# Performance work log

Measured on AMD Instinct MI355X. Metric: run time of the kernel, lower is better.

The kernel has to match this reference:

```python
import jax, jax.numpy as jnp
import numpy as np

K = 64  # hardcoded in MAN.__init__
D_DRUG = 128
D_PROT = 128


def setup_inputs() -> dict:
    key = jax.random.key(0)
    ks = jax.random.split(key, 7)
    B, Ld, Lp = 64, 512, 1024

    def xavier(k, shape):
        fan_in, fan_out = shape[-1], shape[-2]
        std = (2.0 / (fan_in + fan_out)) ** 0.5
        return jax.random.normal(k, shape, dtype=jnp.float32) * std

    return {
        "drug": jax.random.normal(ks[0], (B, Ld, D_DRUG), dtype=jnp.float32),
        "target": jax.random.normal(ks[1], (B, Lp, D_PROT), dtype=jnp.float32),
        "W_b": xavier(ks[2], (D_PROT, D_DRUG)),
        "W_x": xavier(ks[3], (K, D_DRUG)),
        "W_p": xavier(ks[4], (K, D_PROT)),
        "w_hx": xavier(ks[5], (K, 1)),
        "w_hp": xavier(ks[6], (K, 1)),
    }


def reference(drug, target, W_b, W_x, W_p, w_hx, w_hp):
    # drug:   [B, Ld, Dd] ; target: [B, Lp, Dp]
    d = jnp.swapaxes(drug, 1, 2)            # [B, Dd, Ld]  (drug.permute(0,2,1))
    tT = jnp.swapaxes(target, 1, 2)         # [B, Dp, Lp]

    # C = tanh(target @ (W_b @ d))  -> [B, Lp, Ld]
    C = jnp.tanh(jnp.einsum('bpe,ed,bdl->bpl', target, W_b, d))

    Wx_d = jnp.einsum('kd,bdl->bkl', W_x, d)     # [B, k, Ld]
    Wp_t = jnp.einsum('ke,bep->bkp', W_p, tT)    # [B, k, Lp]

    H_c = jnp.tanh(Wx_d + jnp.einsum('bkp,bpl->bkl', Wp_t, C))   # [B, k, Ld]
    H_p = jnp.tanh(Wp_t + jnp.einsum('bkl,bpl->bkp', Wx_d, C))   # [B, k, Lp]

    a_c = jax.nn.softmax(jnp.einsum('k,bkl->bl', w_hx[:, 0], H_c), axis=-1)  # [B, Ld]
    a_p = jax.nn.softmax(jnp.einsum('k,bkp->bp', w_hp[:, 0], H_p), axis=-1)  # [B, Lp]

    c = jnp.einsum('bl,bld->bd', a_c, drug)      # [B, Dd]
    p = jnp.einsum('bp,bpe->be', a_p, target)    # [B, Dp]
    return (c, p)
```

## Files before the change

kernel.cpp:

```cpp
#include <hip/hip_runtime.h>
#include <hip/hip_bf16.h>
#include <math.h>

#define NB 64
#define LD 512
#define LP 1024
#define DD 128
#define KK 64

using half8 = __attribute__((ext_vector_type(8))) _Float16;
using half4 = __attribute__((ext_vector_type(4))) _Float16;
using f32x4 = __attribute__((ext_vector_type(4))) float;

__device__ __forceinline__ float ftanh(float x) {
    float e = __expf(2.0f * x);
    return 1.0f - 2.0f * __builtin_amdgcn_rcpf(e + 1.0f);
}

__global__ void k_conv(const float* __restrict__ in, _Float16* __restrict__ out, int n) {
    int i = (blockIdx.x * blockDim.x + threadIdx.x) * 4;
    int stride = gridDim.x * blockDim.x * 4;
    for (; i < n; i += stride) {
        float4 v = *reinterpret_cast<const float4*>(in + i);
        half4 h;
        h.x = (_Float16)v.x; h.y = (_Float16)v.y; h.z = (_Float16)v.z; h.w = (_Float16)v.w;
        *reinterpret_cast<half4*>(out + i) = h;
    }
}

__global__ void k_prep(const float* __restrict__ Wb, _Float16* __restrict__ WbT,
                       const float* __restrict__ Wx, _Float16* __restrict__ Wx_h,
                       const float* __restrict__ Wp, _Float16* __restrict__ Wp_h)
{
    int bid = blockIdx.x, tid = threadIdx.x;
    if (bid < 64) {
        int t = bid * 256 + tid;
        int d = t >> 7, e = t & 127;
        WbT[t] = (_Float16)Wb[e * 128 + d];
    } else {
        const float* src = (bid < 72) ? Wx : Wp;
        _Float16* dst = (bid < 72) ? Wx_h : Wp_h;
        int i = ((bid & 7) * 256 + tid) * 4;
        float4 v = *reinterpret_cast<const float4*>(src + i);
        half4 h;
        h.x = (_Float16)v.x; h.y = (_Float16)v.y; h.z = (_Float16)v.z; h.w = (_Float16)v.w;
        *reinterpret_cast<half4*>(dst + i) = h;
    }
}

__global__ void k_sentinel(float* out) {
    if (threadIdx.x == 0 && blockIdx.x == 0) out[0] = 1000.0f;
}

__global__ __launch_bounds__(256)
void k_gemm3(const _Float16* __restrict__ drug_h, const _Float16* __restrict__ targ_h,
             const _Float16* __restrict__ WbT_h, const _Float16* __restrict__ Wx_h,
             const _Float16* __restrict__ Wp_h,
             _Float16* __restrict__ tb_h, _Float16* __restrict__ Wxd_h,
             _Float16* __restrict__ Wpt_h)
{
    __shared__ alignas(16) _Float16 smem[64 * 72 + 128 * 72];
    _Float16* As = smem;
    _Float16* Bs = smem + 64 * 72;

    int bid = blockIdx.x;
    const _Float16 *A, *Bm;
    _Float16* Out;
    long sA, sB, sOut;
    int N, tilesN, t;
    const int Kd = 128;
    if (bid < 256)      { A = Wx_h;  sA = 0;            Bm = drug_h; sB = (long)LD * DD; Out = Wxd_h; sOut = (long)KK * LD; N = LD;  tilesN = 4; t = bid; }
    else if (bid < 768) { A = Wp_h;  sA = 0;            Bm = targ_h; sB = (long)LP * DD; Out = Wpt_h; sOut = (long)KK * LP; N = LP;  tilesN = 8; t = bid - 256; }
    else                { A = targ_h; sA = (long)LP * DD; Bm = WbT_h; sB = 0;            Out = tb_h;  sOut = (long)LP * DD; N = 128; tilesN = 1; t = bid - 768; }

    int tpb = (tilesN == 1) ? 16 : tilesN;
    int b = t / tpb;
    int q = t % tpb;
    int m0 = (tilesN == 1) ? q * 64 : 0;
    int n0 = (tilesN == 1) ? 0 : q * 128;

    const _Float16* Ab = A + (long)b * sA;
    const _Float16* Bb = Bm + (long)b * sB;

    int tid = threadIdx.x;
    int lane = tid & 63;
    int wid = tid >> 6;
    int wm = wid & 1, wn = wid >> 1;

    f32x4 acc[2][4];
#pragma unroll
    for (int i = 0; i < 2; i++)
#pragma unroll
        for (int j = 0; j < 4; j++) acc[i][j] = (f32x4)(0.0f);

    for (int k0 = 0; k0 < Kd; k0 += 64) {
#pragma unroll
        for (int i = 0; i < 2; i++) {
            int c = tid + i * 256;
            int row = c >> 3, col = c & 7;
            int4 v = *reinterpret_cast<const int4*>(Ab + (long)(m0 + row) * Kd + k0 + col * 8);
            *reinterpret_cast<int4*>(&As[row * 72 + col * 8]) = v;
        }
#pragma unroll
        for (int i = 0; i < 4; i++) {
            int c = tid + i * 256;
            int row = c >> 3, col = c & 7;
            int4 v = *reinterpret_cast<const int4*>(Bb + (long)(n0 + row) * Kd + k0 + col * 8);
            *reinterpret_cast<int4*>(&Bs[row * 72 + col * 8]) = v;
        }
        __syncthreads();
#pragma unroll
        for (int kk = 0; kk < 64; kk += 32) {
            int klane = kk + 8 * (lane >> 4);
            half8 af[2], bfr[4];
#pragma unroll
            for (int fm = 0; fm < 2; fm++)
                af[fm] = *reinterpret_cast<const half8*>(&As[(wm * 32 + fm * 16 + (lane & 15)) * 72 + klane]);
#pragma unroll
            for (int fn = 0; fn < 4; fn++)
                bfr[fn] = *reinterpret_cast<const half8*>(&Bs[(wn * 64 + fn * 16 + (lane & 15)) * 72 + klane]);
#pragma unroll
            for (int fm = 0; fm < 2; fm++)
#pragma unroll
                for (int fn = 0; fn < 4; fn++)
                    acc[fm][fn] = __builtin_amdgcn_mfma_f32_16x16x32_f16(af[fm], bfr[fn], acc[fm][fn], 0, 0, 0);
        }
        __syncthreads();
    }

    long ob = (long)b * sOut;
#pragma unroll
    for (int fm = 0; fm < 2; fm++)
#pragma unroll
        for (int fn = 0; fn < 4; fn++)
#pragma unroll
            for (int r = 0; r < 4; r++) {
                int row = m0 + wm * 32 + fm * 16 + (lane >> 4) * 4 + r;
                int col = n0 + wn * 64 + fn * 16 + (lane & 15);
                Out[ob + (long)row * N + col] = (_Float16)acc[fm][fn][r];
            }
}

__global__ __launch_bounds__(256)
void k_score_fused(const _Float16* __restrict__ drug_h, const _Float16* __restrict__ tb_h,
                   const _Float16* __restrict__ Wxd_h, const _Float16* __restrict__ Wpt_h,
                   const float* __restrict__ whx, const float* __restrict__ whp,
                   float* __restrict__ sc_c, float* __restrict__ sc_p)
{
    __shared__ alignas(16) _Float16 Ss[64 * 136];
    __shared__ alignas(16) _Float16 Ws[64 * 72];
    __shared__ alignas(16) _Float16 Cts[64 * 72];
    __shared__ float sred[8 * 64];
    __shared__ float wsh[64];

    int P = blockIdx.x;
    int tid = threadIdx.x;
    int lane = tid & 63;
    int wid = tid >> 6;
    int wm = wid & 1, wn = wid >> 1;

    int b, n0, nsteps, Ntot, sW;
    const _Float16 *R, *S, *W, *Add;
    const float* wv;
    float* out;
    if (P < 512) {
        int x = P & 7, j = P >> 3;
        b = x * 8 + (j >> 3);
        n0 = (j & 7) * 64;
        R = drug_h + (long)b * (LD * DD);
        S = tb_h   + (long)b * (LP * DD);
        W = Wpt_h  + (long)b * (KK * LP);  sW = LP;
        Add = Wxd_h + (long)b * (KK * LD); Ntot = LD;
        nsteps = LP / 64; wv = whx; out = sc_c + (long)b * LD;
    } else {
        int Q = P - 512;
        int x = Q & 7, j = Q >> 3;
        b = x * 8 + (j >> 4);
        n0 = (j & 15) * 64;
        R = tb_h   + (long)b * (LP * DD);
        S = drug_h + (long)b * (LD * DD);
        W = Wxd_h  + (long)b * (KK * LD);  sW = LD;
        Add = Wpt_h + (long)b * (KK * LP); Ntot = LP;
        nsteps = LD / 64; wv = whp; out = sc_p + (long)b * LP;
    }

    half8 af[2][4];
#pragma unroll
    for (int fm = 0; fm < 2; fm++)
#pragma unroll
        for (int kk = 0; kk < 4; kk++) {
            int row = n0 + wm * 32 + fm * 16 + (lane & 15);
            int col = kk * 32 + 8 * (lane >> 4);
            af[fm][kk] = *reinterpret_cast<const half8*>(R + (long)row * DD + col);
        }
    if (tid < 64) wsh[tid] = wv[tid];

    f32x4 acc2[2][2];
#pragma unroll
    for (int i = 0; i < 2; i++)
#pragma unroll
        for (int j = 0; j < 2; j++) acc2[i][j] = (f32x4)(0.0f);

    for (int s = 0; s < nsteps; s++) {
        __syncthreads();
#pragma unroll
        for (int i = 0; i < 4; i++) {
            int c = tid + i * 256;
            int row = c >> 4, col8 = (c & 15) * 8;
            int4 v = *reinterpret_cast<const int4*>(S + (long)(s * 64 + row) * DD + col8);
            *reinterpret_cast<int4*>(&Ss[row * 136 + col8]) = v;
        }
#pragma unroll
        for (int i = 0; i < 2; i++) {
            int c = tid + i * 256;
            int row = c >> 3, col8 = (c & 7) * 8;
            int4 v = *reinterpret_cast<const int4*>(W + (long)row * sW + s * 64 + col8);
            *reinterpret_cast<int4*>(&Ws[row * 72 + col8]) = v;
        }
        __syncthreads();

        f32x4 a1[2][2];
#pragma unroll
        for (int i = 0; i < 2; i++)
#pragma unroll
            for (int j = 0; j < 2; j++) a1[i][j] = (f32x4)(0.0f);
#pragma unroll
        for (int kk = 0; kk < 4; kk++) {
            int klane = kk * 32 + 8 * (lane >> 4);
            half8 bf[2];
#pragma unroll
            for (int fn = 0; fn < 2; fn++)
                bf[fn] = *reinterpret_cast<const half8*>(&Ss[(wn * 32 + fn * 16 + (lane & 15)) * 136 + klane]);
#pragma unroll
            for (int fn = 0; fn < 2; fn++)
#pragma unroll
                for (int fm = 0; fm < 2; fm++)
                    a1[fn][fm] = __builtin_amdgcn_mfma_f32_16x16x32_f16(bf[fn], af[fm][kk], a1[fn][fm], 0, 0, 0);
        }
#pragma unroll
        for (int fn = 0; fn < 2; fn++)
#pragma unroll
            for (int fm = 0; fm < 2; fm++) {
                int res   = wm * 32 + fm * 16 + (lane & 15);
                int strm0 = wn * 32 + fn * 16 + 4 * (lane >> 4);
                half4 hv;
                hv.x = (_Float16)ftanh(a1[fn][fm][0]);
                hv.y = (_Float16)ftanh(a1[fn][fm][1]);
                hv.z = (_Float16)ftanh(a1[fn][fm][2]);
                hv.w = (_Float16)ftanh(a1[fn][fm][3]);
                *reinterpret_cast<half4*>(&Cts[res * 72 + strm0]) = hv;
            }
        __syncthreads();

#pragma unroll
        for (int kk = 0; kk < 2; kk++) {
            int klane = kk * 32 + 8 * (lane >> 4);
            half8 aw[2], bf2[2];
#pragma unroll
            for (int fm = 0; fm < 2; fm++)
                aw[fm] = *reinterpret_cast<const half8*>(&Ws[(wm * 32 + fm * 16 + (lane & 15)) * 72 + klane]);
#pragma unroll
            for (int fn = 0; fn < 2; fn++)
                bf2[fn] = *reinterpret_cast<const half8*>(&Cts[(wn * 32 + fn * 16 + (lane & 15)) * 72 + klane]);
#pragma unroll
            for (int fm = 0; fm < 2; fm++)
#pragma unroll
                for (int fn = 0; fn < 2; fn++)
                    acc2[fm][fn] = __builtin_amdgcn_mfma_f32_16x16x32_f16(aw[fm], bf2[fn], acc2[fm][fn], 0, 0, 0);
        }
    }

    float ps[2] = {0.f, 0.f};
#pragma unroll
    for (int fm = 0; fm < 2; fm++)
#pragma unroll
        for (int fn = 0; fn < 2; fn++)
#pragma unroll
            for (int r = 0; r < 4; r++) {
                int k   = wm * 32 + fm * 16 + (lane >> 4) * 4 + r;
                int col = wn * 32 + fn * 16 + (lane & 15);
                float v = ftanh(acc2[fm][fn][r] + (float)Add[(long)k * Ntot + n0 + col]);
                ps[fn] += wsh[k] * v;
            }
#pragma unroll
    for (int fn = 0; fn < 2; fn++)
        sred[(wm * 4 + (lane >> 4)) * 64 + wn * 32 + fn * 16 + (lane & 15)] = ps[fn];
    __syncthreads();
    if (tid < 64) {
        float sacc = 0.f;
#pragma unroll
        for (int j = 0; j < 8; j++) sacc += sred[j * 64 + tid];
        out[n0 + tid] = sacc;
    }
}

__device__ __forceinline__ float wred_max(float v) {
#pragma unroll
    for (int off = 32; off > 0; off >>= 1) v = fmaxf(v, __shfl_xor(v, off, 64));
    return v;
}
__device__ __forceinline__ float wred_sum(float v) {
#pragma unroll
    for (int off = 32; off > 0; off >>= 1) v += __shfl_xor(v, off, 64);
    return v;
}

__global__ __launch_bounds__(1024)
void k_soft(const float* __restrict__ scc, const float* __restrict__ scp,
            float* __restrict__ ac, float* __restrict__ ap)
{
    __shared__ float r16[16];
    int b = blockIdx.x, tid = threadIdx.x;
    int lane = tid & 63, wid = tid >> 6;

    float s = (tid < 512) ? scc[b * 512 + tid] : -3.4e38f;
    float m = wred_max(s);
    if (lane == 0) r16[wid] = m;
    __syncthreads();
    m = r16[0];
#pragma unroll
    for (int i = 1; i < 16; i++) m = fmaxf(m, r16[i]);
    float e = (tid < 512) ? __expf(s - m) : 0.f;
    __syncthreads();
    float t = wred_sum(e);
    if (lane == 0) r16[wid] = t;
    __syncthreads();
    float sum = 0.f;
#pragma unroll
    for (int i = 0; i < 16; i++) sum += r16[i];
    if (tid < 512) ac[b * 512 + tid] = e * __builtin_amdgcn_rcpf(sum);
    __syncthreads();

    float s2 = scp[b * 1024 + tid];
    float m2 = wred_max(s2);
    if (lane == 0) r16[wid] = m2;
    __syncthreads();
    m2 = r16[0];
#pragma unroll
    for (int i = 1; i < 16; i++) m2 = fmaxf(m2, r16[i]);
    float e2 = __expf(s2 - m2);
    __syncthreads();
    float t2 = wred_sum(e2);
    if (lane == 0) r16[wid] = t2;
    __syncthreads();
    float sum2 = 0.f;
#pragma unroll
    for (int i = 0; i < 16; i++) sum2 += r16[i];
    ap[b * 1024 + tid] = e2 * __builtin_amdgcn_rcpf(sum2);
}

__global__ __launch_bounds__(512)
void k_wsum(const _Float16* __restrict__ drug_h, const _Float16* __restrict__ targ_h,
            const float* __restrict__ ac, const float* __restrict__ ap,
            float* __restrict__ out)
{
    __shared__ float ash[1024];
    __shared__ float red[32 * 128];
    int b = blockIdx.x, side = blockIdx.y;
    int L = side ? LP : LD;
    const _Float16* X = side ? targ_h : drug_h;
    const float* a = side ? ap : ac;
    float* ob = out + side * 8192 + b * 128;
    int tid = threadIdx.x;

    for (int i = tid; i < L; i += 512) ash[i] = a[(long)b * L + i];
    __syncthreads();

    int col8 = tid & 15, rg = tid >> 4;
    float accv[8];
#pragma unroll
    for (int j = 0; j < 8; j++) accv[j] = 0.f;
    const _Float16* Xb = X + (long)b * L * 128;
    for (int l = rg; l < L; l += 32) {
        half8 v = *reinterpret_cast<const half8*>(&Xb[l * 128 + col8 * 8]);
        float av = ash[l];
#pragma unroll
        for (int j = 0; j < 8; j++) accv[j] += av * (float)v[j];
    }
#pragma unroll
    for (int j = 0; j < 8; j++) red[rg * 128 + col8 * 8 + j] = accv[j];
    __syncthreads();
    if (tid < 128) {
        float s = 0.f;
#pragma unroll
        for (int g = 0; g < 32; g++) s += red[g * 128 + tid];
        ob[tid] = s;
    }
}

extern "C" void kernel_launch(void* const* d_in, const int* in_sizes, int n_in,
                              void* d_out, int out_size, void* d_ws, size_t ws_size,
                              hipStream_t stream) {
    (void)in_sizes; (void)n_in; (void)out_size;
    const float* drug   = (const float*)d_in[0];
    const float* target = (const float*)d_in[1];
    const float* Wb     = (const float*)d_in[2];
    const float* Wx     = (const float*)d_in[3];
    const float* Wp     = (const float*)d_in[4];
    const float* whx    = (const float*)d_in[5];
    const float* whp    = (const float*)d_in[6];

    char* w = (char*)d_ws;
    size_t off = 0;
    auto takeb = [&](size_t bytes) {
        void* p = (void*)(w + off);
        off += (bytes + 255) & ~(size_t)255;
        return p;
    };
    _Float16* drug_h = (_Float16*)takeb((size_t)NB * LD * DD * 2);
    _Float16* targ_h = (_Float16*)takeb((size_t)NB * LP * DD * 2);
    _Float16* WbT_h  = (_Float16*)takeb(128 * 128 * 2);
    _Float16* Wx_h   = (_Float16*)takeb(64 * 128 * 2);
    _Float16* Wp_h   = (_Float16*)takeb(64 * 128 * 2);
    _Float16* tb_h   = (_Float16*)takeb((size_t)NB * LP * DD * 2);
    _Float16* Wxd_h  = (_Float16*)takeb((size_t)NB * KK * LD * 2);
    _Float16* Wpt_h  = (_Float16*)takeb((size_t)NB * KK * LP * 2);
    float*    sc_c   = (float*)takeb((size_t)NB * LD * 4);
    float*    sc_p   = (float*)takeb((size_t)NB * LP * 4);
    float*    a_c    = (float*)takeb((size_t)NB * LD * 4);
    float*    a_p    = (float*)takeb((size_t)NB * LP * 4);

    if (off > ws_size) {
        k_sentinel<<<1, 64, 0, stream>>>((float*)d_out);
        return;
    }

    k_conv<<<1024, 256, 0, stream>>>(drug,   drug_h, NB * LD * DD);
    k_conv<<<1024, 256, 0, stream>>>(target, targ_h, NB * LP * DD);
    k_prep<<<80, 256, 0, stream>>>(Wb, WbT_h, Wx, Wx_h, Wp, Wp_h);

    k_gemm3<<<dim3(1792), 256, 0, stream>>>(
        drug_h, targ_h, WbT_h, Wx_h, Wp_h, tb_h, Wxd_h, Wpt_h);

    k_score_fused<<<dim3(512 + 1024), 256, 0, stream>>>(
        drug_h, tb_h, Wxd_h, Wpt_h, whx, whp, sc_c, sc_p);

    k_soft<<<NB, 1024, 0, stream>>>(sc_c, sc_p, a_c, a_p);
    k_wsum<<<dim3(NB, 2), 512, 0, stream>>>(drug_h, targ_h, a_c, a_p, (float*)d_out);
}
```

Baseline: 102.5 us.

## Double per-block output tile in fused score kernel to reuse streamed tiles

New measurement: 87.84 us. 1.17x faster.

```diff
diff --git a/kernel.cpp b/kernel.cpp
--- a/kernel.cpp
+++ b/kernel.cpp
@@ -141,7 +141,7 @@
             }
 }
 
-__global__ __launch_bounds__(256)
+__global__ __launch_bounds__(256, 3)
 void k_score_fused(const _Float16* __restrict__ drug_h, const _Float16* __restrict__ tb_h,
                    const _Float16* __restrict__ Wxd_h, const _Float16* __restrict__ Wpt_h,
                    const float* __restrict__ whx, const float* __restrict__ whp,
@@ -149,8 +149,8 @@
 {
     __shared__ alignas(16) _Float16 Ss[64 * 136];
     __shared__ alignas(16) _Float16 Ws[64 * 72];
-    __shared__ alignas(16) _Float16 Cts[64 * 72];
-    __shared__ float sred[8 * 64];
+    __shared__ alignas(16) _Float16 Cts[128 * 72];
+    __shared__ float sred[8 * 128];
     __shared__ float wsh[64];
 
     int P = blockIdx.x;
@@ -163,20 +163,20 @@
     const _Float16 *R, *S, *W, *Add;
     const float* wv;
     float* out;
-    if (P < 512) {
+    if (P < 256) {
         int x = P & 7, j = P >> 3;
-        b = x * 8 + (j >> 3);
-        n0 = (j & 7) * 64;
+        b = x * 8 + (j >> 2);
+        n0 = (j & 3) * 128;
         R = drug_h + (long)b * (LD * DD);
         S = tb_h   + (long)b * (LP * DD);
         W = Wpt_h  + (long)b * (KK * LP);  sW = LP;
         Add = Wxd_h + (long)b * (KK * LD); Ntot = LD;
         nsteps = LP / 64; wv = whx; out = sc_c + (long)b * LD;
     } else {
-        int Q = P - 512;
+        int Q = P - 256;
         int x = Q & 7, j = Q >> 3;
-        b = x * 8 + (j >> 4);
-        n0 = (j & 15) * 64;
+        b = x * 8 + (j >> 3);
+        n0 = (j & 7) * 128;
         R = tb_h   + (long)b * (LP * DD);
         S = drug_h + (long)b * (LD * DD);
         W = Wxd_h  + (long)b * (KK * LD);  sW = LD;
@@ -184,22 +184,22 @@
         nsteps = LD / 64; wv = whp; out = sc_p + (long)b * LP;
     }
 
-    half8 af[2][4];
-#pragma unroll
-    for (int fm = 0; fm < 2; fm++)
+    half8 af[4][4];
+#pragma unroll
+    for (int fm = 0; fm < 4; fm++)
 #pragma unroll
         for (int kk = 0; kk < 4; kk++) {
-            int row = n0 + wm * 32 + fm * 16 + (lane & 15);
+            int row = n0 + wm * 64 + fm * 16 + (lane & 15);
             int col = kk * 32 + 8 * (lane >> 4);
             af[fm][kk] = *reinterpret_cast<const half8*>(R + (long)row * DD + col);
         }
     if (tid < 64) wsh[tid] = wv[tid];
 
-    f32x4 acc2[2][2];
+    f32x4 acc2[2][4];
 #pragma unroll
     for (int i = 0; i < 2; i++)
 #pragma unroll
-        for (int j = 0; j < 2; j++) acc2[i][j] = (f32x4)(0.0f);
+        for (int j = 0; j < 4; j++) acc2[i][j] = (f32x4)(0.0f);
 
     for (int s = 0; s < nsteps; s++) {
         __syncthreads();
@@ -219,11 +219,11 @@
         }
         __syncthreads();
 
-        f32x4 a1[2][2];
+        f32x4 a1[2][4];
 #pragma unroll
         for (int i = 0; i < 2; i++)
 #pragma unroll
-            for (int j = 0; j < 2; j++) a1[i][j] = (f32x4)(0.0f);
+            for (int j = 0; j < 4; j++) a1[i][j] = (f32x4)(0.0f);
 #pragma unroll
         for (int kk = 0; kk < 4; kk++) {
             int klane = kk * 32 + 8 * (lane >> 4);
@@ -234,14 +234,14 @@
 #pragma unroll
             for (int fn = 0; fn < 2; fn++)
 #pragma unroll
-                for (int fm = 0; fm < 2; fm++)
+                for (int fm = 0; fm < 4; fm++)
                     a1[fn][fm] = __builtin_amdgcn_mfma_f32_16x16x32_f16(bf[fn], af[fm][kk], a1[fn][fm], 0, 0, 0);
         }
 #pragma unroll
         for (int fn = 0; fn < 2; fn++)
 #pragma unroll
-            for (int fm = 0; fm < 2; fm++) {
-                int res   = wm * 32 + fm * 16 + (lane & 15);
+            for (int fm = 0; fm < 4; fm++) {
+                int res   = wm * 64 + fm * 16 + (lane & 15);
                 int strm0 = wn * 32 + fn * 16 + 4 * (lane >> 4);
                 half4 hv;
                 hv.x = (_Float16)ftanh(a1[fn][fm][0]);
@@ -255,41 +255,41 @@
 #pragma unroll
         for (int kk = 0; kk < 2; kk++) {
             int klane = kk * 32 + 8 * (lane >> 4);
-            half8 aw[2], bf2[2];
-#pragma unroll
-            for (int fm = 0; fm < 2; fm++)
-                aw[fm] = *reinterpret_cast<const half8*>(&Ws[(wm * 32 + fm * 16 + (lane & 15)) * 72 + klane]);
-#pragma unroll
-            for (int fn = 0; fn < 2; fn++)
-                bf2[fn] = *reinterpret_cast<const half8*>(&Cts[(wn * 32 + fn * 16 + (lane & 15)) * 72 + klane]);
-#pragma unroll
-            for (int fm = 0; fm < 2; fm++)
-#pragma unroll
-                for (int fn = 0; fn < 2; fn++)
-                    acc2[fm][fn] = __builtin_amdgcn_mfma_f32_16x16x32_f16(aw[fm], bf2[fn], acc2[fm][fn], 0, 0, 0);
-        }
-    }
-
-    float ps[2] = {0.f, 0.f};
-#pragma unroll
-    for (int fm = 0; fm < 2; fm++)
-#pragma unroll
-        for (int fn = 0; fn < 2; fn++)
+            half8 aw[2], bf2[4];
+#pragma unroll
+            for (int fm2 = 0; fm2 < 2; fm2++)
+                aw[fm2] = *reinterpret_cast<const half8*>(&Ws[(wm * 32 + fm2 * 16 + (lane & 15)) * 72 + klane]);
+#pragma unroll
+            for (int fn2 = 0; fn2 < 4; fn2++)
+                bf2[fn2] = *reinterpret_cast<const half8*>(&Cts[(wn * 64 + fn2 * 16 + (lane & 15)) * 72 + klane]);
+#pragma unroll
+            for (int fm2 = 0; fm2 < 2; fm2++)
+#pragma unroll
+                for (int fn2 = 0; fn2 < 4; fn2++)
+                    acc2[fm2][fn2] = __builtin_amdgcn_mfma_f32_16x16x32_f16(aw[fm2], bf2[fn2], acc2[fm2][fn2], 0, 0, 0);
+        }
+    }
+
+    float ps[4] = {0.f, 0.f, 0.f, 0.f};
+#pragma unroll
+    for (int fm2 = 0; fm2 < 2; fm2++)
+#pragma unroll
+        for (int fn2 = 0; fn2 < 4; fn2++)
 #pragma unroll
             for (int r = 0; r < 4; r++) {
-                int k   = wm * 32 + fm * 16 + (lane >> 4) * 4 + r;
-                int col = wn * 32 + fn * 16 + (lane & 15);
-                float v = ftanh(acc2[fm][fn][r] + (float)Add[(long)k * Ntot + n0 + col]);
-                ps[fn] += wsh[k] * v;
+                int k   = wm * 32 + fm2 * 16 + (lane >> 4) * 4 + r;
+                int col = wn * 64 + fn2 * 16 + (lane & 15);
+                float v = ftanh(acc2[fm2][fn2][r] + (float)Add[(long)k * Ntot + n0 + col]);
+                ps[fn2] += wsh[k] * v;
             }
 #pragma unroll
-    for (int fn = 0; fn < 2; fn++)
-        sred[(wm * 4 + (lane >> 4)) * 64 + wn * 32 + fn * 16 + (lane & 15)] = ps[fn];
-    __syncthreads();
-    if (tid < 64) {
+    for (int fn2 = 0; fn2 < 4; fn2++)
+        sred[(wm * 4 + (lane >> 4)) * 128 + wn * 64 + fn2 * 16 + (lane & 15)] = ps[fn2];
+    __syncthreads();
+    if (tid < 128) {
         float sacc = 0.f;
 #pragma unroll
-        for (int j = 0; j < 8; j++) sacc += sred[j * 64 + tid];
+        for (int j = 0; j < 8; j++) sacc += sred[j * 128 + tid];
         out[n0 + tid] = sacc;
     }
 }
@@ -432,7 +432,7 @@
     k_gemm3<<<dim3(1792), 256, 0, stream>>>(
         drug_h, targ_h, WbT_h, Wx_h, Wp_h, tb_h, Wxd_h, Wpt_h);
 
-    k_score_fused<<<dim3(512 + 1024), 256, 0, stream>>>(
+    k_score_fused<<<dim3(256 + 512), 256, 0, stream>>>(
         drug_h, tb_h, Wxd_h, Wpt_h, whx, whp, sc_c, sc_p);
 
     k_soft<<<NB, 1024, 0, stream>>>(sc_c, sc_p, a_c, a_p);
```
